# Kernel tuning notes

Measured on AMD Instinct MI355X. Metric: run time of the kernel, lower is better.

The kernel has to match this reference:

```python
import jax, jax.numpy as jnp
import numpy as np

N_NODES = 100000
NEG_SLOPE = 0.2  # DGL GATConv default negative_slope


def gat_layer(x, src, dst, W, attn_l, attn_r, bias, n_nodes):
    """Single-head DGL GATConv. x: [N, in], returns [N, out]."""
    h = x @ W                              # [N, out]  fc (no bias)
    el = h @ attn_l                        # [N]
    er = h @ attn_r                        # [N]
    e = el[src] + er[dst]                  # [E]
    e = jnp.where(e >= 0, e, NEG_SLOPE * e)  # leaky_relu
    # segment softmax over incoming edges of each dst node
    m = jax.ops.segment_max(e, dst, num_segments=n_nodes)   # [N]
    ex = jnp.exp(e - m[dst])                                 # [E]
    s = jax.ops.segment_sum(ex, dst, num_segments=n_nodes)  # [N]
    a = ex / s[dst]                                          # [E]
    # weighted aggregate of source features
    msg = a[:, None] * h[src]                                # [E, out]
    out = jax.ops.segment_sum(msg, dst, num_segments=n_nodes)
    return out + bias


def setup_inputs() -> dict:
    key = jax.random.key(0)
    ks = jax.random.split(key, 12)
    n, e = N_NODES, 1600000
    in_f, hid_f, out_f = 128, 64, 64
    inp = {
        "features": jax.random.normal(ks[0], (n, in_f), dtype=jnp.float32),
        "edge_weights": jax.random.uniform(ks[1], (e,), dtype=jnp.float32),
        "src": jax.random.randint(ks[2], (e,), 0, n, dtype=jnp.int32),
        "dst": jax.random.randint(ks[3], (e,), 0, n, dtype=jnp.int32),
        "W1": jax.random.normal(ks[4], (in_f, hid_f), dtype=jnp.float32) * (1.0 / np.sqrt(in_f)),
        "attn_l1": jax.random.normal(ks[5], (hid_f,), dtype=jnp.float32) * 0.1,
        "attn_r1": jax.random.normal(ks[6], (hid_f,), dtype=jnp.float32) * 0.1,
        "bias1": jnp.zeros((hid_f,), dtype=jnp.float32),
        "W2": jax.random.normal(ks[7], (hid_f, out_f), dtype=jnp.float32) * (1.0 / np.sqrt(hid_f)),
        "attn_l2": jax.random.normal(ks[8], (out_f,), dtype=jnp.float32) * 0.1,
        "attn_r2": jax.random.normal(ks[9], (out_f,), dtype=jnp.float32) * 0.1,
        "bias2": jnp.zeros((out_f,), dtype=jnp.float32),
    }
    return inp


def reference(features, edge_weights, src, dst, W1, attn_l1, attn_r1, bias1,
              W2, attn_l2, attn_r2, bias2):
    n = features.shape[0]
    # conv1 -> DGL returns [N, 1, hid]; relu; conv2 -> [N, 1, 1, out]
    h = gat_layer(features, src, dst, W1, attn_l1, attn_r1, bias1, n)  # [N, hid]
    h = jax.nn.relu(h)
    out = gat_layer(h, src, dst, W2, attn_l2, attn_r2, bias2, n)       # [N, out]
    # edge_weights is accepted but unused, matching the original forward
    return out.reshape(n, 1, 1, -1)
```

## Files before the change

### kernel.cpp

```cpp
#include <hip/hip_runtime.h>
#include <hip/hip_fp16.h>
#include <type_traits>

#define NEG_SLOPE 0.2f
#define BKT_SHIFT 8
#define BKT_SIZE (1 << BKT_SHIFT)
#define BKT_CAP 12288
#define P1_EPT 16

typedef __attribute__((ext_vector_type(8))) short short8;
typedef __attribute__((ext_vector_type(4))) float float4v;

__device__ inline int rfl_i(int v) { return __builtin_amdgcn_readfirstlane(v); }

__device__ inline unsigned short f2bf(float f) {
    unsigned u = __float_as_uint(f);
    unsigned r = u + 0x7FFFu + ((u >> 16) & 1u);
    return (unsigned short)(r >> 16);
}
__device__ inline float bf2f(unsigned short b) {
    return __uint_as_float(((unsigned)b) << 16);
}


__global__ void init_cur(int* __restrict__ gcur, int nbkt) {
    int t = blockIdx.x * blockDim.x + threadIdx.x;
    if (t < nbkt) gcur[t] = t * BKT_CAP;
}

__global__ __launch_bounds__(256) void partition_kernel(
        const int* __restrict__ src, const int* __restrict__ dst, int e,
        int* __restrict__ gcur, int* __restrict__ part, int nbkt) {
    __shared__ int cnt[4][392];
    __shared__ int base_l[4][392];
    int t = threadIdx.x;
    int wv = t >> 6;
    int cb = blockIdx.x * (256 * P1_EPT);
    for (int i = t; i < 4 * 392; i += 256) ((int*)cnt)[i] = 0;
    __syncthreads();
    int sr[P1_EPT], ds[P1_EPT], rk[P1_EPT];
#pragma unroll
    for (int i4 = 0; i4 < P1_EPT / 4; ++i4) {
        int eid0 = cb + (i4 * 256 + t) * 4;
        int4 s4, d4;
        bool full = (eid0 + 3 < e);
        if (full) {
            s4 = *(const int4*)(src + eid0);
            d4 = *(const int4*)(dst + eid0);
        }
#pragma unroll
        for (int j = 0; j < 4; ++j) {
            int i = i4 * 4 + j;
            int eid = eid0 + j;
            if (full) {
                sr[i] = (&s4.x)[j];
                ds[i] = (&d4.x)[j];
            } else if (eid < e) {
                sr[i] = src[eid];
                ds[i] = dst[eid];
            }
            rk[i] = (eid < e) ? atomicAdd(&cnt[wv][ds[i] >> BKT_SHIFT], 1) : -1;
        }
    }
    __syncthreads();
    for (int b = t; b < nbkt; b += 256) {
        int c0 = cnt[0][b], c1 = cnt[1][b], c2 = cnt[2][b], c3 = cnt[3][b];
        int tot = c0 + c1 + c2 + c3;
        if (tot > 0) {
            int gb = atomicAdd(&gcur[b], tot);
            base_l[0][b] = gb;
            base_l[1][b] = gb + c0;
            base_l[2][b] = gb + c0 + c1;
            base_l[3][b] = gb + c0 + c1 + c2;
        }
    }
    __syncthreads();
#pragma unroll
    for (int i = 0; i < P1_EPT; ++i) {
        if (rk[i] >= 0) {
            int b = ds[i] >> BKT_SHIFT;
            part[base_l[wv][b] + rk[i]] = (sr[i] << BKT_SHIFT) | (ds[i] & (BKT_SIZE - 1));
        }
    }
}

__global__ void cnt_scan(const int* __restrict__ gcur, int* __restrict__ bbase,
                         int nbkt, int e_total) {
    __shared__ int tmp[256];
    int t = threadIdx.x;
    int b0 = 2 * t, b1 = 2 * t + 1;
    int c0 = (b0 < nbkt) ? (gcur[b0] - b0 * BKT_CAP) : 0;
    int c1 = (b1 < nbkt) ? (gcur[b1] - b1 * BKT_CAP) : 0;
    int s = c0 + c1;
    tmp[t] = s;
    __syncthreads();
    for (int o = 1; o < 256; o <<= 1) {
        int x = tmp[t];
        int y = (t >= o) ? tmp[t - o] : 0;
        __syncthreads();
        tmp[t] = x + y;
        __syncthreads();
    }
    int excl = tmp[t] - s;
    if (b0 < nbkt) bbase[b0] = excl;
    if (b1 < nbkt) bbase[b1] = excl + c0;
    if (t == 0) bbase[nbkt] = e_total;
}

__global__ __launch_bounds__(256) void finesort2(
        const int* __restrict__ part, const int* __restrict__ gcur,
        const int* __restrict__ bbase, int* __restrict__ row_off,
        int* __restrict__ csr_src, int n, int e_total, int nbkt) {
    __shared__ int cnt[BKT_SIZE];
    __shared__ int cur[BKT_SIZE];
    __shared__ int tmp[BKT_SIZE];
    int b = blockIdx.x, t = threadIdx.x;
    int d0 = b << BKT_SHIFT;
    int nloc = min(BKT_SIZE, n - d0);
    cnt[t] = 0;
    __syncthreads();
    int abase = b * BKT_CAP, aend = gcur[b];
    for (int i = abase + t; i < aend; i += 256)
        atomicAdd(&cnt[part[i] & (BKT_SIZE - 1)], 1);
    __syncthreads();
    int c = cnt[t];
    tmp[t] = c;
    __syncthreads();
    for (int o = 1; o < 256; o <<= 1) {
        int x = tmp[t];
        int y = (t >= o) ? tmp[t - o] : 0;
        __syncthreads();
        tmp[t] = x + y;
        __syncthreads();
    }
    int pos0 = bbase[b] + tmp[t] - c;
    cur[t] = pos0;
    if (t < nloc) row_off[d0 + t] = pos0;
    if (b == nbkt - 1 && t == 0) row_off[n] = e_total;
    __syncthreads();
    for (int i = abase + t; i < aend; i += 256) {
        int pk = part[i];
        int pos = atomicAdd(&cur[pk & (BKT_SIZE - 1)], 1);
        csr_src[pos] = ((unsigned)pk) >> BKT_SHIFT;
    }
}

__global__ void wprep_kernel(const float* __restrict__ W, unsigned short* __restrict__ wh,
                             unsigned short* __restrict__ wl, int K) {
    int idx = blockIdx.x * blockDim.x + threadIdx.x;
    int KT = K / 32;
    if (idx >= KT * 4 * 64) return;
    int lane = idx & 63;
    int fbkt = idx >> 6;
    int fb = fbkt & 3, kt = fbkt >> 2;
    int q = lane >> 4, c = lane & 15;
    for (int j = 0; j < 8; ++j) {
        float w = W[(kt * 32 + q * 8 + j) * 64 + fb * 16 + c];
        unsigned short hi = f2bf(w);
        wh[idx * 8 + j] = hi;
        wl[idx * 8 + j] = f2bf(w - bf2f(hi));
    }
}

template <int KT, typename IN>
__global__ __launch_bounds__(256) void gemm_mfma_kernel(
        const IN* __restrict__ x, const unsigned short* __restrict__ wh,
        const unsigned short* __restrict__ wl,
        const float* __restrict__ al, const float* __restrict__ ar,
        __half* __restrict__ h16, float* __restrict__ el,
        float* __restrict__ er, int n) {
    constexpr int K = KT * 32;
    constexpr int WFRAG = KT * 4 * 64 * 8;
    __shared__ unsigned short Wh[WFRAG];
    __shared__ unsigned short Wl[WFRAG];
    for (int i = threadIdx.x; i < WFRAG / 8; i += 256) {
        ((float4*)Wh)[i] = ((const float4*)wh)[i];
        ((float4*)Wl)[i] = ((const float4*)wl)[i];
    }
    __syncthreads();

    int lane = threadIdx.x & 63;
    int q = lane >> 4, c = lane & 15;
    int wave = (int)((blockIdx.x * blockDim.x + threadIdx.x) >> 6);
    int nwaves = (gridDim.x * blockDim.x) >> 6;
    int ntiles = (n + 15) >> 4;

    float alv[4], arv[4];
#pragma unroll
    for (int fb = 0; fb < 4; ++fb) {
        alv[fb] = al[fb * 16 + c];
        arv[fb] = ar[fb * 16 + c];
    }

    for (int t = wave; t < ntiles; t += nwaves) {
        int v0 = t * 16;
        int row = min(v0 + c, n - 1);
        const IN* xr = x + (size_t)row * K + q * 8;

        short8 Ah[KT], Al[KT];
#pragma unroll
        for (int kt = 0; kt < KT; ++kt) {
            float xv[8];
            if constexpr (std::is_same<IN, float>::value) {
                *(float4*)&xv[0] = *(const float4*)(xr + kt * 32);
                *(float4*)&xv[4] = *(const float4*)(xr + kt * 32 + 4);
            } else {
                __half hh[8];
                *(uint4*)hh = *(const uint4*)(xr + kt * 32);
#pragma unroll
                for (int j = 0; j < 8; ++j) xv[j] = __half2float(hh[j]);
            }
#pragma unroll
            for (int j = 0; j < 8; ++j) {
                unsigned short hi = f2bf(xv[j]);
                Ah[kt][j] = (short)hi;
                Al[kt][j] = (short)f2bf(xv[j] - bf2f(hi));
            }
        }

        float4v acc[4];
#pragma unroll
        for (int fb = 0; fb < 4; ++fb) acc[fb] = (float4v)0.f;

#pragma unroll
        for (int kt = 0; kt < KT; ++kt) {
#pragma unroll
            for (int fb = 0; fb < 4; ++fb) {
                short8 bh = *(const short8*)&Wh[((kt * 4 + fb) * 64 + lane) * 8];
                short8 bl = *(const short8*)&Wl[((kt * 4 + fb) * 64 + lane) * 8];
                acc[fb] = __builtin_amdgcn_mfma_f32_16x16x32_bf16(Ah[kt], bh, acc[fb], 0, 0, 0);
                acc[fb] = __builtin_amdgcn_mfma_f32_16x16x32_bf16(Al[kt], bh, acc[fb], 0, 0, 0);
                acc[fb] = __builtin_amdgcn_mfma_f32_16x16x32_bf16(Ah[kt], bl, acc[fb], 0, 0, 0);
            }
        }

#pragma unroll
        for (int r = 0; r < 4; ++r) {
            int v = v0 + q * 4 + r;
            float pl = 0.f, pr = 0.f;
            bool ok = (v < n);
#pragma unroll
            for (int fb = 0; fb < 4; ++fb) {
                float hv = acc[fb][r];
                if (ok) h16[(size_t)v * 64 + fb * 16 + c] = __float2half(hv);
                pl = fmaf(hv, alv[fb], pl);
                pr = fmaf(hv, arv[fb], pr);
            }
#pragma unroll
            for (int off = 8; off > 0; off >>= 1) {
                pl += __shfl_xor(pl, off);
                pr += __shfl_xor(pr, off);
            }
            if (ok && c == 0) { el[v] = pl; er[v] = pr; }
        }
    }
}

template <typename OUT>
__global__ __launch_bounds__(256) void agg_kernel(
        const int* __restrict__ row_off, const int* __restrict__ csr_src,
        const __half* __restrict__ h16, const float* __restrict__ el,
        const float* __restrict__ er, const float* __restrict__ bias,
        OUT* __restrict__ out, int n, int do_relu) {
    int lane = threadIdx.x & 63;
    int grp = lane >> 4;
    int c = lane & 15;
    int gwave = rfl_i((int)((blockIdx.x * blockDim.x + threadIdx.x) >> 6));
    int nwaves = (gridDim.x * blockDim.x) >> 6;
    float4 b4 = ((const float4*)bias)[c];
    for (int v = gwave; v < n; v += nwaves) {
        int rs = rfl_i(row_off[v]), re = rfl_i(row_off[v + 1]);
        float er_v = er[v];
        float a0 = 0.f, a1 = 0.f, a2 = 0.f, a3 = 0.f, ssum = 0.f;
        for (int base = rs; base < re; base += 64) {
            int cnt = min(64, re - base);
            int s_e = 0;
            float ex = 0.f;
            if (lane < cnt) {
                s_e = csr_src[base + lane];
                float ev = el[s_e] + er_v;
                ev = (ev >= 0.f) ? ev : NEG_SLOPE * ev;
                ex = __expf(ev);
            }
            float cs = ex;
#pragma unroll
            for (int off = 32; off > 0; off >>= 1) cs += __shfl_xor(cs, off);
            ssum += cs;
            int cnt16 = (cnt + 15) & ~15;
            for (int j = 0; j < cnt16; j += 16) {
                int sj[4];
                float exj[4];
                uint2 hv[4];
#pragma unroll
                for (int u = 0; u < 4; ++u) {
                    int idx = j + 4 * u + grp;
                    sj[u] = __shfl(s_e, idx);
                    exj[u] = __shfl(ex, idx);
                    hv[u] = *((const uint2*)(h16 + (size_t)sj[u] * 64) + c);
                }
#pragma unroll
                for (int u = 0; u < 4; ++u) {
                    float2 f01 = __half22float2(*(__half2*)&hv[u].x);
                    float2 f23 = __half22float2(*(__half2*)&hv[u].y);
                    a0 = fmaf(exj[u], f01.x, a0);
                    a1 = fmaf(exj[u], f01.y, a1);
                    a2 = fmaf(exj[u], f23.x, a2);
                    a3 = fmaf(exj[u], f23.y, a3);
                }
            }
        }
#pragma unroll
        for (int off = 16; off < 64; off <<= 1) {
            a0 += __shfl_xor(a0, off);
            a1 += __shfl_xor(a1, off);
            a2 += __shfl_xor(a2, off);
            a3 += __shfl_xor(a3, off);
        }
        if (lane < 16) {
            float4 o;
            if (re > rs) {
                float inv = 1.0f / ssum;
                o.x = fmaf(a0, inv, b4.x);
                o.y = fmaf(a1, inv, b4.y);
                o.z = fmaf(a2, inv, b4.z);
                o.w = fmaf(a3, inv, b4.w);
            } else {
                o = b4;
            }
            if (do_relu) {
                o.x = fmaxf(o.x, 0.f);
                o.y = fmaxf(o.y, 0.f);
                o.z = fmaxf(o.z, 0.f);
                o.w = fmaxf(o.w, 0.f);
            }
            if constexpr (std::is_same<OUT, __half>::value) {
                uint2 pk;
                *(__half2*)&pk.x = __float22half2_rn(make_float2(o.x, o.y));
                *(__half2*)&pk.y = __float22half2_rn(make_float2(o.z, o.w));
                ((uint2*)(out + (size_t)v * 64))[c] = pk;
            } else {
                ((float4*)(out + (size_t)v * 64))[c] = o;
            }
        }
    }
}

extern "C" void kernel_launch(void* const* d_in, const int* in_sizes, int n_in,
                              void* d_out, int out_size, void* d_ws, size_t ws_size,
                              hipStream_t stream) {
    (void)n_in; (void)out_size; (void)ws_size;
    const float* features = (const float*)d_in[0];
    const int*   src = (const int*)d_in[2];
    const int*   dst = (const int*)d_in[3];
    const float* W1  = (const float*)d_in[4];
    const float* al1 = (const float*)d_in[5];
    const float* ar1 = (const float*)d_in[6];
    const float* b1  = (const float*)d_in[7];
    const float* W2  = (const float*)d_in[8];
    const float* al2 = (const float*)d_in[9];
    const float* ar2 = (const float*)d_in[10];
    const float* b2  = (const float*)d_in[11];

    const int n = in_sizes[0] / 128;
    const int e = in_sizes[2];
    float* out = (float*)d_out;

    char* p = (char*)d_ws;
    auto alloc = [&](size_t bytes) -> char* {
        char* q = p;
        p += (bytes + 255) & ~(size_t)255;
        return q;
    };
    int*    row_off = (int*)alloc((size_t)(n + 1) * 4);
    int*    csr_src = (int*)alloc((size_t)e * 4);
    __half* h16     = (__half*)alloc((size_t)n * 64 * 2);
    __half* hr      = (__half*)alloc((size_t)n * 64 * 2);
    float*  el      = (float*)alloc((size_t)n * 4);
    float*  er      = (float*)alloc((size_t)n * 4);
    int*    gcur    = (int*)alloc(512 * 4);
    int*    bbase   = (int*)alloc(513 * 4);
    unsigned short* w1h = (unsigned short*)alloc(4 * 4 * 64 * 8 * 2);
    unsigned short* w1l = (unsigned short*)alloc(4 * 4 * 64 * 8 * 2);
    unsigned short* w2h = (unsigned short*)alloc(2 * 4 * 64 * 8 * 2);
    unsigned short* w2l = (unsigned short*)alloc(2 * 4 * 64 * 8 * 2);
    int*    part    = (int*)h16;

    const int nbkt = (n + BKT_SIZE - 1) >> BKT_SHIFT;

    wprep_kernel<<<4, 256, 0, stream>>>(W1, w1h, w1l, 128);
    wprep_kernel<<<2, 256, 0, stream>>>(W2, w2h, w2l, 64);

    init_cur<<<2, 256, 0, stream>>>(gcur, nbkt);
    partition_kernel<<<(e + 256 * P1_EPT - 1) / (256 * P1_EPT), 256, 0, stream>>>(
        src, dst, e, gcur, part, nbkt);
    cnt_scan<<<1, 256, 0, stream>>>(gcur, bbase, nbkt, e);
    finesort2<<<nbkt, 256, 0, stream>>>(part, gcur, bbase, row_off, csr_src, n, e, nbkt);

    gemm_mfma_kernel<4, float><<<512, 256, 0, stream>>>(features, w1h, w1l, al1, ar1,
                                                        h16, el, er, n);
    agg_kernel<__half><<<4096, 256, 0, stream>>>(row_off, csr_src, h16, el, er, b1, hr, n, 1);

    gemm_mfma_kernel<2, __half><<<512, 256, 0, stream>>>(hr, w2h, w2l, al2, ar2,
                                                         h16, el, er, n);
    agg_kernel<float><<<4096, 256, 0, stream>>>(row_off, csr_src, h16, el, er, b2, out, n, 0);
}
```

Baseline: 253.0 us.

## Fuse edge partition with layer-1 GEMM and fold scan and weight prep into kernels

The edge partition pass and the first projection GEMM now run as one heterogeneous launch, with blocks split by index between the two independent jobs. The bucket-base scan is folded into the fine sort, where each block reduces the counts of the preceding buckets itself. Weight bf16 hi/lo splitting moves into each GEMM block's prologue, and the init kernel is replaced by a memset. The partition scratch moves into the output buffer so it no longer aliases h16. The aim is to cut launch count and let the partition and GEMM overlap, at the cost of redundant per-block weight conversion and bucket reduction.

Result: faster. 244.3 us (-3.4%).

```diff
diff --git a/kernel.cpp b/kernel.cpp
--- a/kernel.cpp
+++ b/kernel.cpp
@@ -22,20 +22,15 @@
     return __uint_as_float(((unsigned)b) << 16);
 }
 
-
-__global__ void init_cur(int* __restrict__ gcur, int nbkt) {
-    int t = blockIdx.x * blockDim.x + threadIdx.x;
-    if (t < nbkt) gcur[t] = t * BKT_CAP;
-}
-
-__global__ __launch_bounds__(256) void partition_kernel(
+__device__ __forceinline__ void partition_body(
         const int* __restrict__ src, const int* __restrict__ dst, int e,
-        int* __restrict__ gcur, int* __restrict__ part, int nbkt) {
-    __shared__ int cnt[4][392];
-    __shared__ int base_l[4][392];
+        int* __restrict__ gcur, int* __restrict__ part, int nbkt, int b_id,
+        char* smem) {
+    int (*cnt)[392]    = (int(*)[392])smem;
+    int (*base_l)[392] = (int(*)[392])(smem + 4 * 392 * sizeof(int));
     int t = threadIdx.x;
     int wv = t >> 6;
-    int cb = blockIdx.x * (256 * P1_EPT);
+    int cb = b_id * (256 * P1_EPT);
     for (int i = t; i < 4 * 392; i += 256) ((int*)cnt)[i] = 0;
     __syncthreads();
     int sr[P1_EPT], ds[P1_EPT], rk[P1_EPT];
@@ -67,7 +62,7 @@
         int c0 = cnt[0][b], c1 = cnt[1][b], c2 = cnt[2][b], c3 = cnt[3][b];
         int tot = c0 + c1 + c2 + c3;
         if (tot > 0) {
-            int gb = atomicAdd(&gcur[b], tot);
+            int gb = b * BKT_CAP + atomicAdd(&gcur[b], tot);
             base_l[0][b] = gb;
             base_l[1][b] = gb + c0;
             base_l[2][b] = gb + c0 + c1;
@@ -84,15 +79,36 @@
     }
 }
 
-__global__ void cnt_scan(const int* __restrict__ gcur, int* __restrict__ bbase,
-                         int nbkt, int e_total) {
-    __shared__ int tmp[256];
-    int t = threadIdx.x;
-    int b0 = 2 * t, b1 = 2 * t + 1;
-    int c0 = (b0 < nbkt) ? (gcur[b0] - b0 * BKT_CAP) : 0;
-    int c1 = (b1 < nbkt) ? (gcur[b1] - b1 * BKT_CAP) : 0;
-    int s = c0 + c1;
-    tmp[t] = s;
+__global__ __launch_bounds__(256) void finesort3(
+        const int* __restrict__ part, const int* __restrict__ gcur,
+        int* __restrict__ row_off, int* __restrict__ csr_src,
+        int n, int e_total, int nbkt) {
+    __shared__ int cnt[BKT_SIZE];
+    __shared__ int cur[BKT_SIZE];
+    __shared__ int tmp[BKT_SIZE];
+    int b = blockIdx.x, t = threadIdx.x;
+    int i1 = 256 + t;
+    int v0 = (t < b) ? gcur[t] : 0;
+    int v1 = (i1 < b) ? gcur[i1] : 0;
+    tmp[t] = v0 + v1;
+    __syncthreads();
+    for (int o = 128; o > 0; o >>= 1) {
+        if (t < o) tmp[t] += tmp[t + o];
+        __syncthreads();
+    }
+    int bbase_b = tmp[0];
+    __syncthreads();
+
+    int d0 = b << BKT_SHIFT;
+    int nloc = min(BKT_SIZE, n - d0);
+    cnt[t] = 0;
+    __syncthreads();
+    int abase = b * BKT_CAP, aend = abase + gcur[b];
+    for (int i = abase + t; i < aend; i += 256)
+        atomicAdd(&cnt[part[i] & (BKT_SIZE - 1)], 1);
+    __syncthreads();
+    int c = cnt[t];
+    tmp[t] = c;
     __syncthreads();
     for (int o = 1; o < 256; o <<= 1) {
         int x = tmp[t];
@@ -101,39 +117,7 @@
         tmp[t] = x + y;
         __syncthreads();
     }
-    int excl = tmp[t] - s;
-    if (b0 < nbkt) bbase[b0] = excl;
-    if (b1 < nbkt) bbase[b1] = excl + c0;
-    if (t == 0) bbase[nbkt] = e_total;
-}
-
-__global__ __launch_bounds__(256) void finesort2(
-        const int* __restrict__ part, const int* __restrict__ gcur,
-        const int* __restrict__ bbase, int* __restrict__ row_off,
-        int* __restrict__ csr_src, int n, int e_total, int nbkt) {
-    __shared__ int cnt[BKT_SIZE];
-    __shared__ int cur[BKT_SIZE];
-    __shared__ int tmp[BKT_SIZE];
-    int b = blockIdx.x, t = threadIdx.x;
-    int d0 = b << BKT_SHIFT;
-    int nloc = min(BKT_SIZE, n - d0);
-    cnt[t] = 0;
-    __syncthreads();
-    int abase = b * BKT_CAP, aend = gcur[b];
-    for (int i = abase + t; i < aend; i += 256)
-        atomicAdd(&cnt[part[i] & (BKT_SIZE - 1)], 1);
-    __syncthreads();
-    int c = cnt[t];
-    tmp[t] = c;
-    __syncthreads();
-    for (int o = 1; o < 256; o <<= 1) {
-        int x = tmp[t];
-        int y = (t >= o) ? tmp[t - o] : 0;
-        __syncthreads();
-        tmp[t] = x + y;
-        __syncthreads();
-    }
-    int pos0 = bbase[b] + tmp[t] - c;
+    int pos0 = bbase_b + tmp[t] - c;
     cur[t] = pos0;
     if (t < nloc) row_off[d0 + t] = pos0;
     if (b == nbkt - 1 && t == 0) row_off[n] = e_total;
@@ -145,44 +129,34 @@
     }
 }
 
-__global__ void wprep_kernel(const float* __restrict__ W, unsigned short* __restrict__ wh,
-                             unsigned short* __restrict__ wl, int K) {
-    int idx = blockIdx.x * blockDim.x + threadIdx.x;
-    int KT = K / 32;
-    if (idx >= KT * 4 * 64) return;
-    int lane = idx & 63;
-    int fbkt = idx >> 6;
-    int fb = fbkt & 3, kt = fbkt >> 2;
-    int q = lane >> 4, c = lane & 15;
-    for (int j = 0; j < 8; ++j) {
-        float w = W[(kt * 32 + q * 8 + j) * 64 + fb * 16 + c];
-        unsigned short hi = f2bf(w);
-        wh[idx * 8 + j] = hi;
-        wl[idx * 8 + j] = f2bf(w - bf2f(hi));
-    }
-}
-
 template <int KT, typename IN>
-__global__ __launch_bounds__(256) void gemm_mfma_kernel(
-        const IN* __restrict__ x, const unsigned short* __restrict__ wh,
-        const unsigned short* __restrict__ wl,
+__device__ __forceinline__ void gemm_body(
+        const IN* __restrict__ x, const float* __restrict__ W,
         const float* __restrict__ al, const float* __restrict__ ar,
         __half* __restrict__ h16, float* __restrict__ el,
-        float* __restrict__ er, int n) {
+        float* __restrict__ er, int n, int bid, int nblocks, char* smem) {
     constexpr int K = KT * 32;
     constexpr int WFRAG = KT * 4 * 64 * 8;
-    __shared__ unsigned short Wh[WFRAG];
-    __shared__ unsigned short Wl[WFRAG];
-    for (int i = threadIdx.x; i < WFRAG / 8; i += 256) {
-        ((float4*)Wh)[i] = ((const float4*)wh)[i];
-        ((float4*)Wl)[i] = ((const float4*)wl)[i];
+    unsigned short* Wh = (unsigned short*)smem;
+    unsigned short* Wl = Wh + WFRAG;
+    for (int idx = threadIdx.x; idx < KT * 4 * 64; idx += 256) {
+        int lane = idx & 63, fbkt = idx >> 6;
+        int fb = fbkt & 3, kt = fbkt >> 2;
+        int q = lane >> 4, c = lane & 15;
+#pragma unroll
+        for (int j = 0; j < 8; ++j) {
+            float w = W[(kt * 32 + q * 8 + j) * 64 + fb * 16 + c];
+            unsigned short hi = f2bf(w);
+            Wh[idx * 8 + j] = hi;
+            Wl[idx * 8 + j] = f2bf(w - bf2f(hi));
+        }
     }
     __syncthreads();
 
     int lane = threadIdx.x & 63;
     int q = lane >> 4, c = lane & 15;
-    int wave = (int)((blockIdx.x * blockDim.x + threadIdx.x) >> 6);
-    int nwaves = (gridDim.x * blockDim.x) >> 6;
+    int wave = bid * 4 + (int)(threadIdx.x >> 6);
+    int nwaves = nblocks * 4;
     int ntiles = (n + 15) >> 4;
 
     float alv[4], arv[4];
@@ -254,6 +228,33 @@
             if (ok && c == 0) { el[v] = pl; er[v] = pr; }
         }
     }
+}
+
+__global__ __launch_bounds__(256) void part_gemm1(
+        const int* __restrict__ src, const int* __restrict__ dst, int e,
+        int* __restrict__ gcur, int* __restrict__ part, int nbkt, int npb,
+        const float* __restrict__ x, const float* __restrict__ W1,
+        const float* __restrict__ al, const float* __restrict__ ar,
+        __half* __restrict__ h16, float* __restrict__ el,
+        float* __restrict__ er, int n) {
+    __shared__ char smem[32768];
+    int b = (int)blockIdx.x;
+    if (b < npb)
+        partition_body(src, dst, e, gcur, part, nbkt, b, smem);
+    else
+        gemm_body<4, float>(x, W1, al, ar, h16, el, er, n, b - npb,
+                            (int)gridDim.x - npb, smem);
+}
+
+template <int KT, typename IN>
+__global__ __launch_bounds__(256) void gemm_mfma_kernel(
+        const IN* __restrict__ x, const float* __restrict__ W,
+        const float* __restrict__ al, const float* __restrict__ ar,
+        __half* __restrict__ h16, float* __restrict__ el,
+        float* __restrict__ er, int n) {
+    __shared__ char smem[KT * 4 * 64 * 8 * 2 * 2];
+    gemm_body<KT, IN>(x, W, al, ar, h16, el, er, n, (int)blockIdx.x,
+                      (int)gridDim.x, smem);
 }
 
 template <typename OUT>
@@ -378,29 +379,19 @@
     float*  el      = (float*)alloc((size_t)n * 4);
     float*  er      = (float*)alloc((size_t)n * 4);
     int*    gcur    = (int*)alloc(512 * 4);
-    int*    bbase   = (int*)alloc(513 * 4);
-    unsigned short* w1h = (unsigned short*)alloc(4 * 4 * 64 * 8 * 2);
-    unsigned short* w1l = (unsigned short*)alloc(4 * 4 * 64 * 8 * 2);
-    unsigned short* w2h = (unsigned short*)alloc(2 * 4 * 64 * 8 * 2);
-    unsigned short* w2l = (unsigned short*)alloc(2 * 4 * 64 * 8 * 2);
-    int*    part    = (int*)h16;
+    int*    part    = (int*)d_out;
 
     const int nbkt = (n + BKT_SIZE - 1) >> BKT_SHIFT;
-
-    wprep_kernel<<<4, 256, 0, stream>>>(W1, w1h, w1l, 128);
-    wprep_kernel<<<2, 256, 0, stream>>>(W2, w2h, w2l, 64);
-
-    init_cur<<<2, 256, 0, stream>>>(gcur, nbkt);
-    partition_kernel<<<(e + 256 * P1_EPT - 1) / (256 * P1_EPT), 256, 0, stream>>>(
-        src, dst, e, gcur, part, nbkt);
-    cnt_scan<<<1, 256, 0, stream>>>(gcur, bbase, nbkt, e);
-    finesort2<<<nbkt, 256, 0, stream>>>(part, gcur, bbase, row_off, csr_src, n, e, nbkt);
-
-    gemm_mfma_kernel<4, float><<<512, 256, 0, stream>>>(features, w1h, w1l, al1, ar1,
-                                                        h16, el, er, n);
+    const int npb  = (e + 256 * P1_EPT - 1) / (256 * P1_EPT);
+
+    hipMemsetAsync(gcur, 0, 512 * sizeof(int), stream);
+
+    part_gemm1<<<npb + 512, 256, 0, stream>>>(src, dst, e, gcur, part, nbkt, npb,
+                                              features, W1, al1, ar1, h16, el, er, n);
+    finesort3<<<nbkt, 256, 0, stream>>>(part, gcur, row_off, csr_src, n, e, nbkt);
+
     agg_kernel<__half><<<4096, 256, 0, stream>>>(row_off, csr_src, h16, el, er, b1, hr, n, 1);
 
-    gemm_mfma_kernel<2, __half><<<512, 256, 0, stream>>>(hr, w2h, w2l, al2, ar2,
-                                                         h16, el, er, n);
+    gemm_mfma_kernel<2, __half><<<512, 256, 0, stream>>>(hr, W2, al2, ar2, h16, el, er, n);
     agg_kernel<float><<<4096, 256, 0, stream>>>(row_off, csr_src, h16, el, er, b2, out, n, 0);
 }
```
